# Kernel tuning notes

Measured on AMD Instinct MI355X. Metric: run time of the kernel, lower is better.

Reference implementation:

```python
import jax, jax.numpy as jnp
import numpy as np

B, S, IN, H, D, STATE, PRED = 256, 512, 32, 256, 32, 4, 96


def setup_inputs() -> dict:
    key = jax.random.key(0)
    ks = jax.random.split(key, 16)
    sc = 1.0 / np.sqrt(H)

    def u(k, shape):
        return jax.random.uniform(k, shape, jnp.float32, -sc, sc)

    return {
        "x": jax.random.normal(ks[0], (B, S, IN), jnp.float32),
        # GRU layer 0
        "W_ih_l0": u(ks[1], (3 * H, IN)),
        "W_hh_l0": u(ks[2], (3 * H, H)),
        "b_ih_l0": u(ks[3], (3 * H,)),
        "b_hh_l0": u(ks[4], (3 * H,)),
        # GRU layer 1
        "W_ih_l1": u(ks[5], (3 * H, H)),
        "W_hh_l1": u(ks[6], (3 * H, H)),
        "b_ih_l1": u(ks[7], (3 * H,)),
        "b_hh_l1": u(ks[8], (3 * H,)),
        # state projection: hidden -> STATE*output_dim
        "W_proj": u(ks[9], (STATE * D, H)),
        "b_proj": u(ks[10], (STATE * D,)),
        # observation matrix, eye-initialized (output_dim, STATE)
        "C": jnp.eye(D, STATE, dtype=jnp.float32),
        "raw_level_decay": jnp.zeros((D,), jnp.float32),
        "raw_trend_decay": jnp.zeros((D,), jnp.float32),
        "raw_gamma": jnp.zeros((D,), jnp.float32),
        "omega": jnp.zeros((D,), jnp.float32),
    }


def _gru_layer(xs, W_ih, W_hh, b_ih, b_hh):
    # xs: (B, S, in_dim). Precompute input projections as one big GEMM.
    xp = jnp.einsum('bsi,gi->bsg', xs, W_ih) + b_ih  # (B, S, 3H)

    def step(h, xt):
        gh = h @ W_hh.T + b_hh  # (B, 3H)
        xr, xz, xn = jnp.split(xt, 3, axis=-1)
        hr, hz, hn = jnp.split(gh, 3, axis=-1)
        r = jax.nn.sigmoid(xr + hr)
        z = jax.nn.sigmoid(xz + hz)
        n = jnp.tanh(xn + r * hn)
        h_new = (1.0 - z) * n + z * h
        return h_new, h_new

    h0 = jnp.zeros((xs.shape[0], W_hh.shape[1]), xs.dtype)
    _, hs = jax.lax.scan(step, h0, jnp.swapaxes(xp, 0, 1))  # (S, B, H)
    return jnp.swapaxes(hs, 0, 1)  # (B, S, H)


def reference(x, W_ih_l0, W_hh_l0, b_ih_l0, b_hh_l0,
              W_ih_l1, W_hh_l1, b_ih_l1, b_hh_l1,
              W_proj, b_proj, C,
              raw_level_decay, raw_trend_decay, raw_gamma, omega):
    h1 = _gru_layer(x, W_ih_l0, W_hh_l0, b_ih_l0, b_hh_l0)
    h2 = _gru_layer(h1, W_ih_l1, W_hh_l1, b_ih_l1, b_hh_l1)
    final_h = h2[:, -1, :]  # (B, H)

    d_out = C.shape[0]
    s = (final_h @ W_proj.T + b_proj).reshape(x.shape[0], d_out, STATE)  # (B, D, 4)

    # time-invariant block-diagonal transition coefficients
    a_l = jax.nn.sigmoid(raw_level_decay) * 0.15 + 0.85
    a_t = jax.nn.sigmoid(raw_trend_decay) * 0.25 + 0.7
    g = jax.nn.sigmoid(raw_gamma) * 0.2 + 0.8
    c, sn = jnp.cos(omega), jnp.sin(omega)
    rot00, rot01 = g * c, -g * sn
    rot10, rot11 = g * sn, g * c

    def step(s, _):
        new_s = jnp.stack([
            s[..., 0] * a_l,
            s[..., 1] * a_t,
            s[..., 2] * rot00 + s[..., 3] * rot10,
            s[..., 2] * rot01 + s[..., 3] * rot11,
        ], axis=-1)
        y = jnp.einsum('ds,bds->bd', C, new_s)
        return new_s, y

    _, ys = jax.lax.scan(step, s, None, length=PRED)  # (PRED, B, D)
    return jnp.swapaxes(ys, 0, 1)  # (B, PRED, D)
```

## Files before the change

### kernel.cpp

```cpp
#include <hip/hip_runtime.h>
#include <cstdio>
#include <cstdint>

typedef _Float16 f16;
typedef f16 hf2   __attribute__((ext_vector_type(2)));
typedef f16 f16x8 __attribute__((ext_vector_type(8)));
typedef float f32x4 __attribute__((ext_vector_type(4)));
typedef unsigned int   u32;
typedef unsigned short u16;

#define B_    256
#define S_    512
#define IN_   32
#define H_    256
#define G3_   768
#define D_    32
#define PRED_ 96
#define TC_   32
#define KPAD_ 72

#if __has_builtin(__builtin_amdgcn_fdot2)
__device__ __forceinline__ float fdot2(hf2 a, hf2 b, float c) {
  return __builtin_amdgcn_fdot2(a, b, c, false);
}
#else
__device__ __forceinline__ float fdot2(hf2 a, hf2 b, float c) {
  return c + (float)a[0] * (float)b[0] + (float)a[1] * (float)b[1];
}
#endif

__device__ __forceinline__ float sigm(float x) {
  return __builtin_amdgcn_rcpf(1.f + __expf(-x));
}
__device__ __forceinline__ float tanh_fast(float x) {
  return 1.f - 2.f * __builtin_amdgcn_rcpf(__expf(2.f * x) + 1.f);
}
__device__ __forceinline__ hf2 bc2(u32 v) { return __builtin_bit_cast(hf2, v); }

__global__ void f32_to_f16_k(const float* __restrict__ in, f16* __restrict__ out, int n) {
  int i = blockIdx.x * blockDim.x + threadIdx.x;
  if (i < n) out[i] = (f16)in[i];
}

__global__ void make_bias(const float* __restrict__ bih, const float* __restrict__ bhh,
                          float* __restrict__ out) {
  int i = blockIdx.x * blockDim.x + threadIdx.x;
  if (i < G3_) out[i] = bih[i] + (i < 512 ? bhh[i] : 0.f);
}

__device__ __forceinline__ f16x8 cvt8(const float* p) {
  float4 lo = ((const float4*)p)[0];
  float4 hi = ((const float4*)p)[1];
  f16x8 r;
  r[0] = (f16)lo.x; r[1] = (f16)lo.y; r[2] = (f16)lo.z; r[3] = (f16)lo.w;
  r[4] = (f16)hi.x; r[5] = (f16)hi.y; r[6] = (f16)hi.z; r[7] = (f16)hi.w;
  return r;
}

template <int KK>
__global__ __launch_bounds__(256) void gemm_xp(
    const void* __restrict__ Asrc, size_t aBlk, int tl_rows,
    const f16* __restrict__ Wih,
    const float* __restrict__ biasc,
    u16* __restrict__ xp) {
  const int tid = threadIdx.x;
  const int wv = tid >> 6, lane = tid & 63, lm = lane & 15, q = lane >> 4;
  const int tiles_pb = tl_rows >> 6;
  const int b = blockIdx.x / tiles_pb, hf = blockIdx.x % tiles_pb;
  const size_t arow0 = (size_t)b * aBlk + (size_t)(hf * 64) * KK;
  const size_t orow0 = (size_t)b * tl_rows + hf * 64;

#pragma unroll 1
  for (int nt = 0; nt < 12; ++nt) {
    const int n0 = wv * 192 + nt * 16;
    const f16* Bp = Wih + (size_t)(n0 + lm) * KK + q * 8;
    f32x4 acc[4];
#pragma unroll
    for (int j = 0; j < 4; ++j) acc[j] = f32x4{0.f, 0.f, 0.f, 0.f};
#pragma unroll
    for (int k0 = 0; k0 < KK; k0 += 32) {
      f16x8 bv = *(const f16x8*)(Bp + k0);
#pragma unroll
      for (int j = 0; j < 4; ++j) {
        f16x8 av;
        if constexpr (KK == 32) {
          av = cvt8((const float*)Asrc + arow0 + (size_t)(j * 16 + lm) * KK + k0 + q * 8);
        } else {
          av = *(const f16x8*)((const f16*)Asrc + arow0 + (size_t)(j * 16 + lm) * KK + k0 + q * 8);
        }
        acc[j] = __builtin_amdgcn_mfma_f32_16x16x32_f16(av, bv, acc[j], 0, 0, 0);
      }
    }
    const float bb = biasc[n0 + lm];
#pragma unroll
    for (int j = 0; j < 4; ++j)
#pragma unroll
      for (int r = 0; r < 4; ++r)
        xp[(orow0 + j * 16 + q * 4 + r) * G3_ + n0 + lm] =
            __builtin_bit_cast(u16, (f16)(acc[j][r] + bb));
  }
}

template <int LAYER>
__global__ __attribute__((amdgpu_flat_work_group_size(1024, 1024)))
__attribute__((amdgpu_waves_per_eu(4, 4))) void gru_rec(
    const u16* __restrict__ xp,
    const f16* __restrict__ Whh16,
    const float* __restrict__ bhh,
    float* __restrict__ hstate,
    f16* __restrict__ h1c,
    int tl_rows, int first) {
  const int b   = blockIdx.x;
  const int tid = threadIdx.x;
  const int p = tid >> 2, kh = tid & 3;

  uint4 w[24];
  const uint4* wsrc = (const uint4*)Whh16 + (size_t)p * 32 + kh * 8;
#pragma unroll
  for (int g = 0; g < 3; ++g)
#pragma unroll
    for (int u = 0; u < 8; ++u)
      w[g * 8 + u] = wsrc[g * 8192 + u];
  const float bhn = bhh[512 + p];

  __shared__ u16 xbuf[2][TC_ * G3_];
  __shared__ __align__(16) u16 hbuf[2][4 * KPAD_];
  __shared__ u16 hhist[TC_ * H_];

  float h = first ? 0.f : hstate[b * H_ + p];
  if (kh == 0)
    hbuf[0][(p >> 6) * KPAD_ + (p & 63)] = __builtin_bit_cast(u16, (f16)h);
  int cur = 0;
  const uint4* xsrc = (const uint4*)xp + (size_t)b * tl_rows * 96;
  const int nsub = tl_rows >> 5;

#pragma unroll 1
  for (int c2 = 0; c2 < nsub; ++c2) {
    {
      const uint4* src = xsrc + (size_t)c2 * 3072;
      uint4 v0 = src[tid], v1 = src[1024 + tid], v2 = src[2048 + tid];
      uint4* dst = (uint4*)xbuf[c2 & 1];
      dst[tid] = v0; dst[1024 + tid] = v1; dst[2048 + tid] = v2;
    }
    __syncthreads();
    const u16* xrow0 = xbuf[c2 & 1];

#pragma unroll 1
    for (int tl = 0; tl < TC_; ++tl) {
      const uint4* hb = (const uint4*)((const u16*)hbuf[cur] + kh * KPAD_);
      float ar = 0.f, az = 0.f, an = 0.f;
#pragma unroll
      for (int cc = 0; cc < 8; ++cc) {
        uint4 hv = hb[cc];
        uint4 w0 = w[cc], w1 = w[8 + cc], w2 = w[16 + cc];
        ar = fdot2(bc2(w0.x), bc2(hv.x), ar);
        az = fdot2(bc2(w1.x), bc2(hv.x), az);
        an = fdot2(bc2(w2.x), bc2(hv.x), an);
        ar = fdot2(bc2(w0.y), bc2(hv.y), ar);
        az = fdot2(bc2(w1.y), bc2(hv.y), az);
        an = fdot2(bc2(w2.y), bc2(hv.y), an);
        ar = fdot2(bc2(w0.z), bc2(hv.z), ar);
        az = fdot2(bc2(w1.z), bc2(hv.z), az);
        an = fdot2(bc2(w2.z), bc2(hv.z), an);
        ar = fdot2(bc2(w0.w), bc2(hv.w), ar);
        az = fdot2(bc2(w1.w), bc2(hv.w), az);
        an = fdot2(bc2(w2.w), bc2(hv.w), an);
      }
      ar += __shfl_xor(ar, 1); ar += __shfl_xor(ar, 2);
      az += __shfl_xor(az, 1); az += __shfl_xor(az, 2);
      an += __shfl_xor(an, 1); an += __shfl_xor(an, 2);

      const u16* xrow = xrow0 + tl * G3_;
      float xr = (float)__builtin_bit_cast(f16, xrow[p]);
      float xz = (float)__builtin_bit_cast(f16, xrow[256 + p]);
      float xn = (float)__builtin_bit_cast(f16, xrow[512 + p]);
      float r = sigm(xr + ar);
      float z = sigm(xz + az);
      float n = tanh_fast(xn + r * (an + bhn));
      h = n + z * (h - n);

      if (kh == 0) {
        u16 h16v = __builtin_bit_cast(u16, (f16)h);
        hbuf[cur ^ 1][(p >> 6) * KPAD_ + (p & 63)] = h16v;
        if constexpr (LAYER == 0) hhist[tl * H_ + p] = h16v;
      }
      __syncthreads();
      cur ^= 1;
    }

    if constexpr (LAYER == 0) {
      uint4 hv = ((const uint4*)hhist)[tid];
      ((uint4*)(h1c + ((size_t)b * tl_rows + c2 * TC_) * H_))[tid] = hv;
    }
  }
  if (kh == 0) hstate[b * H_ + p] = h;
}

__global__ __launch_bounds__(128) void proj_rollout(
    const float* __restrict__ hfinal, const float* __restrict__ Wp,
    const float* __restrict__ bp, const float* __restrict__ Cm,
    const float* __restrict__ rld, const float* __restrict__ rtd,
    const float* __restrict__ rg, const float* __restrict__ om,
    float* __restrict__ out) {
  const int b = blockIdx.x, tid = threadIdx.x;
  __shared__ float fh[256];
  __shared__ float sb[128];
  ((float2*)fh)[tid] = ((const float2*)(hfinal + b * 256))[tid];
  __syncthreads();
  const float4* wrow = (const float4*)(Wp + tid * 256);
  float acc = 0.f;
#pragma unroll 16
  for (int k4 = 0; k4 < 64; k4++) {
    float4 wv = wrow[k4];
    acc += wv.x * fh[4 * k4] + wv.y * fh[4 * k4 + 1] + wv.z * fh[4 * k4 + 2] +
           wv.w * fh[4 * k4 + 3];
  }
  sb[tid] = acc + bp[tid];
  __syncthreads();
  if (tid < 32) {
    const int dd = tid;
    float s0 = sb[dd * 4], s1 = sb[dd * 4 + 1], s2 = sb[dd * 4 + 2], s3 = sb[dd * 4 + 3];
    float al = sigm(rld[dd]) * 0.15f + 0.85f;
    float at = sigm(rtd[dd]) * 0.25f + 0.70f;
    float g  = sigm(rg[dd]) * 0.20f + 0.80f;
    float cw = cosf(om[dd]), sw = sinf(om[dd]);
    float r00 = g * cw, r01 = -g * sw, r10 = g * sw, r11 = g * cw;
    float c0 = Cm[dd * 4], c1 = Cm[dd * 4 + 1], c2 = Cm[dd * 4 + 2], c3 = Cm[dd * 4 + 3];
    float* op = out + (size_t)b * PRED_ * D_ + dd;
    for (int t = 0; t < PRED_; t++) {
      float n0 = s0 * al, n1 = s1 * at;
      float n2 = s2 * r00 + s3 * r10;
      float n3 = s2 * r01 + s3 * r11;
      op[(size_t)t * D_] = c0 * n0 + c1 * n1 + c2 * n2 + c3 * n3;
      s0 = n0; s1 = n1; s2 = n2; s3 = n3;
    }
  }
}

extern "C" void kernel_launch(void* const* d_in, const int* in_sizes, int n_in,
                              void* d_out, int out_size, void* d_ws,
                              size_t ws_size, hipStream_t stream) {
  (void)in_sizes; (void)n_in; (void)out_size;
  const float* x     = (const float*)d_in[0];
  const float* Wih0  = (const float*)d_in[1];
  const float* Whh0  = (const float*)d_in[2];
  const float* bih0  = (const float*)d_in[3];
  const float* bhh0  = (const float*)d_in[4];
  const float* Wih1  = (const float*)d_in[5];
  const float* Whh1  = (const float*)d_in[6];
  const float* bih1  = (const float*)d_in[7];
  const float* bhh1  = (const float*)d_in[8];
  const float* Wproj = (const float*)d_in[9];
  const float* bproj = (const float*)d_in[10];
  const float* Cm    = (const float*)d_in[11];
  const float* rld   = (const float*)d_in[12];
  const float* rtd   = (const float*)d_in[13];
  const float* rg    = (const float*)d_in[14];
  const float* om    = (const float*)d_in[15];
  float* out = (float*)d_out;

  char* ws = (char*)d_ws;
  const size_t wi0_off  = 0;
  const size_t wi1_off  = 49152;
  const size_t whh0_off = 442368;
  const size_t whh1_off = 835584;
  const size_t b0_off   = 1228800;
  const size_t b1_off   = 1231872;
  const size_t hs0_off  = 1234944;
  const size_t hs1_off  = 1497088;
  const size_t h1c_off  = 1759232;
  const size_t need64  = h1c_off + (size_t)B_ * 64 * H_ * 2  + (size_t)B_ * 64 * G3_ * 2;
  const size_t need128 = h1c_off + (size_t)B_ * 128 * H_ * 2 + (size_t)B_ * 128 * G3_ * 2;

  if (ws_size < need64) {
    fprintf(stderr, "kernel_launch: ws too small: have %zu need %zu — skipping\n",
            ws_size, need64);
    return;
  }
  const int TL = (ws_size >= need128) ? 128 : 64;
  const size_t xpc_off = h1c_off + (size_t)B_ * TL * H_ * 2;

  f16* wi016   = (f16*)(ws + wi0_off);
  f16* wi116   = (f16*)(ws + wi1_off);
  f16* whh016  = (f16*)(ws + whh0_off);
  f16* whh116  = (f16*)(ws + whh1_off);
  float* bias0 = (float*)(ws + b0_off);
  float* bias1 = (float*)(ws + b1_off);
  float* hst0  = (float*)(ws + hs0_off);
  float* hst1  = (float*)(ws + hs1_off);
  f16* h1c     = (f16*)(ws + h1c_off);
  u16* xpc     = (u16*)(ws + xpc_off);

  f32_to_f16_k<<<96, 256, 0, stream>>>(Wih0, wi016, G3_ * IN_);
  f32_to_f16_k<<<768, 256, 0, stream>>>(Wih1, wi116, G3_ * H_);
  f32_to_f16_k<<<768, 256, 0, stream>>>(Whh0, whh016, G3_ * H_);
  f32_to_f16_k<<<768, 256, 0, stream>>>(Whh1, whh116, G3_ * H_);
  make_bias<<<3, 256, 0, stream>>>(bih0, bhh0, bias0);
  make_bias<<<3, 256, 0, stream>>>(bih1, bhh1, bias1);

  const int nchunks = S_ / TL;
  const int gblocks = B_ * (TL / 64);
  for (int c = 0; c < nchunks; ++c) {
    gemm_xp<IN_><<<gblocks, 256, 0, stream>>>(
        (const void*)(x + (size_t)c * TL * IN_), (size_t)S_ * IN_, TL, wi016, bias0, xpc);
    gru_rec<0><<<B_, 1024, 0, stream>>>(xpc, whh016, bhh0, hst0, h1c, TL, c == 0);
    gemm_xp<H_><<<gblocks, 256, 0, stream>>>(
        (const void*)h1c, (size_t)TL * H_, TL, wi116, bias1, xpc);
    gru_rec<1><<<B_, 1024, 0, stream>>>(xpc, whh116, bhh1, hst1, nullptr, TL, c == 0);
  }
  proj_rollout<<<B_, 128, 0, stream>>>(hst1, Wproj, bproj, Cm, rld, rtd, rg, om, out);
}
```

Measured before the change: 1.687 ms.

## Halve GRU recurrence block to 512 threads with 2-way K split

Each hidden unit is now handled by 2 threads instead of 4, each holding half of the unit's recurrent weight row (48 uint4 registers instead of 24), with blocks of 512 threads. This removes one shuffle stage per gate and halves the number of waves meeting at each per-step barrier. Two independent accumulator chains per gate are added to shorten dependency latency. The cost is double the weight registers per thread, which risks spills or lower occupancy, and the padded h buffer layout is replaced by a plain contiguous one, which may bring LDS bank conflicts.

```diff
diff --git a/kernel.cpp b/kernel.cpp
--- a/kernel.cpp
+++ b/kernel.cpp
@@ -17,7 +17,6 @@
 #define D_    32
 #define PRED_ 96
 #define TC_   32
-#define KPAD_ 72
 
 #if __has_builtin(__builtin_amdgcn_fdot2)
 __device__ __forceinline__ float fdot2(hf2 a, hf2 b, float c) {
@@ -102,8 +101,7 @@
 }
 
 template <int LAYER>
-__global__ __attribute__((amdgpu_flat_work_group_size(1024, 1024)))
-__attribute__((amdgpu_waves_per_eu(4, 4))) void gru_rec(
+__global__ __launch_bounds__(512, 2) void gru_rec(
     const u16* __restrict__ xp,
     const f16* __restrict__ Whh16,
     const float* __restrict__ bhh,
@@ -112,24 +110,23 @@
     int tl_rows, int first) {
   const int b   = blockIdx.x;
   const int tid = threadIdx.x;
-  const int p = tid >> 2, kh = tid & 3;
-
-  uint4 w[24];
-  const uint4* wsrc = (const uint4*)Whh16 + (size_t)p * 32 + kh * 8;
+  const int p = tid >> 1, kh = tid & 1;
+
+  uint4 w[48];
+  const uint4* wsrc = (const uint4*)Whh16 + (size_t)p * 32 + kh * 16;
 #pragma unroll
   for (int g = 0; g < 3; ++g)
 #pragma unroll
-    for (int u = 0; u < 8; ++u)
-      w[g * 8 + u] = wsrc[g * 8192 + u];
+    for (int u = 0; u < 16; ++u)
+      w[g * 16 + u] = wsrc[g * 8192 + u];
   const float bhn = bhh[512 + p];
 
   __shared__ u16 xbuf[2][TC_ * G3_];
-  __shared__ __align__(16) u16 hbuf[2][4 * KPAD_];
+  __shared__ __align__(16) u16 hbuf[2][H_];
   __shared__ u16 hhist[TC_ * H_];
 
   float h = first ? 0.f : hstate[b * H_ + p];
-  if (kh == 0)
-    hbuf[0][(p >> 6) * KPAD_ + (p & 63)] = __builtin_bit_cast(u16, (f16)h);
+  if (kh == 0) hbuf[0][p] = __builtin_bit_cast(u16, (f16)h);
   int cur = 0;
   const uint4* xsrc = (const uint4*)xp + (size_t)b * tl_rows * 96;
   const int nsub = tl_rows >> 5;
@@ -138,37 +135,40 @@
   for (int c2 = 0; c2 < nsub; ++c2) {
     {
       const uint4* src = xsrc + (size_t)c2 * 3072;
-      uint4 v0 = src[tid], v1 = src[1024 + tid], v2 = src[2048 + tid];
+      uint4 v0 = src[tid],        v1 = src[512 + tid],  v2 = src[1024 + tid];
+      uint4 v3 = src[1536 + tid], v4 = src[2048 + tid], v5 = src[2560 + tid];
       uint4* dst = (uint4*)xbuf[c2 & 1];
-      dst[tid] = v0; dst[1024 + tid] = v1; dst[2048 + tid] = v2;
+      dst[tid] = v0;        dst[512 + tid] = v1;  dst[1024 + tid] = v2;
+      dst[1536 + tid] = v3; dst[2048 + tid] = v4; dst[2560 + tid] = v5;
     }
     __syncthreads();
     const u16* xrow0 = xbuf[c2 & 1];
 
 #pragma unroll 1
     for (int tl = 0; tl < TC_; ++tl) {
-      const uint4* hb = (const uint4*)((const u16*)hbuf[cur] + kh * KPAD_);
-      float ar = 0.f, az = 0.f, an = 0.f;
-#pragma unroll
-      for (int cc = 0; cc < 8; ++cc) {
+      const uint4* hb = (const uint4*)(hbuf[cur] + kh * 128);
+      float ar = 0.f, az = 0.f, an = 0.f, ar2 = 0.f, az2 = 0.f, an2 = 0.f;
+#pragma unroll
+      for (int cc = 0; cc < 16; ++cc) {
         uint4 hv = hb[cc];
-        uint4 w0 = w[cc], w1 = w[8 + cc], w2 = w[16 + cc];
-        ar = fdot2(bc2(w0.x), bc2(hv.x), ar);
-        az = fdot2(bc2(w1.x), bc2(hv.x), az);
-        an = fdot2(bc2(w2.x), bc2(hv.x), an);
-        ar = fdot2(bc2(w0.y), bc2(hv.y), ar);
-        az = fdot2(bc2(w1.y), bc2(hv.y), az);
-        an = fdot2(bc2(w2.y), bc2(hv.y), an);
-        ar = fdot2(bc2(w0.z), bc2(hv.z), ar);
-        az = fdot2(bc2(w1.z), bc2(hv.z), az);
-        an = fdot2(bc2(w2.z), bc2(hv.z), an);
-        ar = fdot2(bc2(w0.w), bc2(hv.w), ar);
-        az = fdot2(bc2(w1.w), bc2(hv.w), az);
-        an = fdot2(bc2(w2.w), bc2(hv.w), an);
+        uint4 w0 = w[cc], w1 = w[16 + cc], w2 = w[32 + cc];
+        ar  = fdot2(bc2(w0.x), bc2(hv.x), ar);
+        az  = fdot2(bc2(w1.x), bc2(hv.x), az);
+        an  = fdot2(bc2(w2.x), bc2(hv.x), an);
+        ar2 = fdot2(bc2(w0.y), bc2(hv.y), ar2);
+        az2 = fdot2(bc2(w1.y), bc2(hv.y), az2);
+        an2 = fdot2(bc2(w2.y), bc2(hv.y), an2);
+        ar  = fdot2(bc2(w0.z), bc2(hv.z), ar);
+        az  = fdot2(bc2(w1.z), bc2(hv.z), az);
+        an  = fdot2(bc2(w2.z), bc2(hv.z), an);
+        ar2 = fdot2(bc2(w0.w), bc2(hv.w), ar2);
+        az2 = fdot2(bc2(w1.w), bc2(hv.w), az2);
+        an2 = fdot2(bc2(w2.w), bc2(hv.w), an2);
       }
-      ar += __shfl_xor(ar, 1); ar += __shfl_xor(ar, 2);
-      az += __shfl_xor(az, 1); az += __shfl_xor(az, 2);
-      an += __shfl_xor(an, 1); an += __shfl_xor(an, 2);
+      ar += ar2; az += az2; an += an2;
+      ar += __shfl_xor(ar, 1);
+      az += __shfl_xor(az, 1);
+      an += __shfl_xor(an, 1);
 
       const u16* xrow = xrow0 + tl * G3_;
       float xr = (float)__builtin_bit_cast(f16, xrow[p]);
@@ -181,7 +181,7 @@
 
       if (kh == 0) {
         u16 h16v = __builtin_bit_cast(u16, (f16)h);
-        hbuf[cur ^ 1][(p >> 6) * KPAD_ + (p & 63)] = h16v;
+        hbuf[cur ^ 1][p] = h16v;
         if constexpr (LAYER == 0) hhist[tl * H_ + p] = h16v;
       }
       __syncthreads();
@@ -189,8 +189,11 @@
     }
 
     if constexpr (LAYER == 0) {
-      uint4 hv = ((const uint4*)hhist)[tid];
-      ((uint4*)(h1c + ((size_t)b * tl_rows + c2 * TC_) * H_))[tid] = hv;
+      uint4 hv0 = ((const uint4*)hhist)[tid];
+      uint4 hv1 = ((const uint4*)hhist)[512 + tid];
+      uint4* dst = (uint4*)(h1c + ((size_t)b * tl_rows + c2 * TC_) * H_);
+      dst[tid] = hv0;
+      dst[512 + tid] = hv1;
     }
   }
   if (kh == 0) hstate[b * H_ + p] = h;
@@ -303,10 +306,10 @@
   for (int c = 0; c < nchunks; ++c) {
     gemm_xp<IN_><<<gblocks, 256, 0, stream>>>(
         (const void*)(x + (size_t)c * TL * IN_), (size_t)S_ * IN_, TL, wi016, bias0, xpc);
-    gru_rec<0><<<B_, 1024, 0, stream>>>(xpc, whh016, bhh0, hst0, h1c, TL, c == 0);
+    gru_rec<0><<<B_, 512, 0, stream>>>(xpc, whh016, bhh0, hst0, h1c, TL, c == 0);
     gemm_xp<H_><<<gblocks, 256, 0, stream>>>(
         (const void*)h1c, (size_t)TL * H_, TL, wi116, bias1, xpc);
-    gru_rec<1><<<B_, 1024, 0, stream>>>(xpc, whh116, bhh1, hst1, nullptr, TL, c == 0);
+    gru_rec<1><<<B_, 512, 0, stream>>>(xpc, whh116, bhh1, hst1, nullptr, TL, c == 0);
   }
   proj_rollout<<<B_, 128, 0, stream>>>(hst1, Wproj, bproj, Cm, rld, rtd, rg, om, out);
 }
```

Measured after the change: 1.555 ms. -7.8%, faster.

## Batch 16 sequences per block and compute GRU recurrence with MFMA

Applied to the files above, without the earlier changes.

Replaces the per-sequence fdot2 recurrent kernel with one where each block processes 16 batch rows and computes the hidden-to-hidden matvec as 16x16x32 MFMA tiles with weights held in registers. Input projections are staged four timesteps at a time into LDS and layer-0 outputs are written directly to global. This aims to use matrix cores instead of scalar dot products, but launches only 16 blocks, leaving most CUs idle and lengthening per-step dependent MFMA chains.

```diff
diff --git a/kernel.cpp b/kernel.cpp
--- a/kernel.cpp
+++ b/kernel.cpp
@@ -16,18 +16,7 @@
 #define G3_   768
 #define D_    32
 #define PRED_ 96
-#define TC_   32
-#define KPAD_ 72
-
-#if __has_builtin(__builtin_amdgcn_fdot2)
-__device__ __forceinline__ float fdot2(hf2 a, hf2 b, float c) {
-  return __builtin_amdgcn_fdot2(a, b, c, false);
-}
-#else
-__device__ __forceinline__ float fdot2(hf2 a, hf2 b, float c) {
-  return c + (float)a[0] * (float)b[0] + (float)a[1] * (float)b[1];
-}
-#endif
+#define XBPAD_ 776
 
 __device__ __forceinline__ float sigm(float x) {
   return __builtin_amdgcn_rcpf(1.f + __expf(-x));
@@ -35,7 +24,6 @@
 __device__ __forceinline__ float tanh_fast(float x) {
   return 1.f - 2.f * __builtin_amdgcn_rcpf(__expf(2.f * x) + 1.f);
 }
-__device__ __forceinline__ hf2 bc2(u32 v) { return __builtin_bit_cast(hf2, v); }
 
 __global__ void f32_to_f16_k(const float* __restrict__ in, f16* __restrict__ out, int n) {
   int i = blockIdx.x * blockDim.x + threadIdx.x;
@@ -102,98 +90,120 @@
 }
 
 template <int LAYER>
-__global__ __attribute__((amdgpu_flat_work_group_size(1024, 1024)))
-__attribute__((amdgpu_waves_per_eu(4, 4))) void gru_rec(
+__global__ __launch_bounds__(512, 2) void gru_rec_mfma(
     const u16* __restrict__ xp,
     const f16* __restrict__ Whh16,
     const float* __restrict__ bhh,
     float* __restrict__ hstate,
     f16* __restrict__ h1c,
-    int tl_rows, int first) {
-  const int b   = blockIdx.x;
+    int TL, int first) {
   const int tid = threadIdx.x;
-  const int p = tid >> 2, kh = tid & 3;
-
-  uint4 w[24];
-  const uint4* wsrc = (const uint4*)Whh16 + (size_t)p * 32 + kh * 8;
-#pragma unroll
-  for (int g = 0; g < 3; ++g)
-#pragma unroll
-    for (int u = 0; u < 8; ++u)
-      w[g * 8 + u] = wsrc[g * 8192 + u];
-  const float bhn = bhh[512 + p];
-
-  __shared__ u16 xbuf[2][TC_ * G3_];
-  __shared__ __align__(16) u16 hbuf[2][4 * KPAD_];
-  __shared__ u16 hhist[TC_ * H_];
-
-  float h = first ? 0.f : hstate[b * H_ + p];
-  if (kh == 0)
-    hbuf[0][(p >> 6) * KPAD_ + (p & 63)] = __builtin_bit_cast(u16, (f16)h);
+  const int wv = tid >> 6, lane = tid & 63, lm = lane & 15, q = lane >> 4;
+  const int b0 = blockIdx.x * 16;
+
+  f16x8 bf[2][3][8];
+#pragma unroll
+  for (int t2 = 0; t2 < 2; ++t2)
+#pragma unroll
+    for (int g = 0; g < 3; ++g)
+#pragma unroll
+      for (int kf = 0; kf < 8; ++kf) {
+        const int u = wv * 32 + t2 * 16 + lm;
+        bf[t2][g][kf] =
+            *(const f16x8*)(Whh16 + (size_t)(g * 256 + u) * 256 + kf * 32 + q * 8);
+      }
+  float bhn[2];
+  bhn[0] = bhh[512 + wv * 32 + lm];
+  bhn[1] = bhh[512 + wv * 32 + 16 + lm];
+
+  __shared__ __align__(16) u16 hlds[2][16][264];
+  __shared__ __align__(16) u16 xb[4][16][XBPAD_];
+
+  float hreg[8];
+#pragma unroll
+  for (int t2 = 0; t2 < 2; ++t2)
+#pragma unroll
+    for (int r = 0; r < 4; ++r) {
+      const int row = q * 4 + r, u = wv * 32 + t2 * 16 + lm;
+      float hv = first ? 0.f : hstate[(size_t)(b0 + row) * 256 + u];
+      hreg[t2 * 4 + r] = hv;
+      hlds[0][row][u] = __builtin_bit_cast(u16, (f16)hv);
+    }
   int cur = 0;
-  const uint4* xsrc = (const uint4*)xp + (size_t)b * tl_rows * 96;
-  const int nsub = tl_rows >> 5;
+  const uint4* gsrc = (const uint4*)xp;
 
 #pragma unroll 1
-  for (int c2 = 0; c2 < nsub; ++c2) {
-    {
-      const uint4* src = xsrc + (size_t)c2 * 3072;
-      uint4 v0 = src[tid], v1 = src[1024 + tid], v2 = src[2048 + tid];
-      uint4* dst = (uint4*)xbuf[c2 & 1];
-      dst[tid] = v0; dst[1024 + tid] = v1; dst[2048 + tid] = v2;
+  for (int t0 = 0; t0 < TL; t0 += 4) {
+#pragma unroll
+    for (int pass = 0; pass < 4; ++pass) {
+      uint4 v[3];
+#pragma unroll
+      for (int i = 0; i < 3; ++i) {
+        const int idx = (pass * 3 + i) * 512 + tid;
+        const int oh = idx * 8;
+        const int s = oh / 12288, rem = oh - s * 12288;
+        const int row = rem / 768, u = rem - row * 768;
+        v[i] = gsrc[(((size_t)(b0 + row) * TL + (t0 + s)) * G3_ + u) >> 3];
+      }
+#pragma unroll
+      for (int i = 0; i < 3; ++i) {
+        const int idx = (pass * 3 + i) * 512 + tid;
+        const int oh = idx * 8;
+        const int s = oh / 12288, rem = oh - s * 12288;
+        const int row = rem / 768, u = rem - row * 768;
+        *(uint4*)(&xb[s][row][u]) = v[i];
+      }
     }
     __syncthreads();
-    const u16* xrow0 = xbuf[c2 & 1];
 
 #pragma unroll 1
-    for (int tl = 0; tl < TC_; ++tl) {
-      const uint4* hb = (const uint4*)((const u16*)hbuf[cur] + kh * KPAD_);
-      float ar = 0.f, az = 0.f, an = 0.f;
-#pragma unroll
-      for (int cc = 0; cc < 8; ++cc) {
-        uint4 hv = hb[cc];
-        uint4 w0 = w[cc], w1 = w[8 + cc], w2 = w[16 + cc];
-        ar = fdot2(bc2(w0.x), bc2(hv.x), ar);
-        az = fdot2(bc2(w1.x), bc2(hv.x), az);
-        an = fdot2(bc2(w2.x), bc2(hv.x), an);
-        ar = fdot2(bc2(w0.y), bc2(hv.y), ar);
-        az = fdot2(bc2(w1.y), bc2(hv.y), az);
-        an = fdot2(bc2(w2.y), bc2(hv.y), an);
-        ar = fdot2(bc2(w0.z), bc2(hv.z), ar);
-        az = fdot2(bc2(w1.z), bc2(hv.z), az);
-        an = fdot2(bc2(w2.z), bc2(hv.z), an);
-        ar = fdot2(bc2(w0.w), bc2(hv.w), ar);
-        az = fdot2(bc2(w1.w), bc2(hv.w), az);
-        an = fdot2(bc2(w2.w), bc2(hv.w), an);
-      }
-      ar += __shfl_xor(ar, 1); ar += __shfl_xor(ar, 2);
-      az += __shfl_xor(az, 1); az += __shfl_xor(az, 2);
-      an += __shfl_xor(an, 1); an += __shfl_xor(an, 2);
-
-      const u16* xrow = xrow0 + tl * G3_;
-      float xr = (float)__builtin_bit_cast(f16, xrow[p]);
-      float xz = (float)__builtin_bit_cast(f16, xrow[256 + p]);
-      float xn = (float)__builtin_bit_cast(f16, xrow[512 + p]);
-      float r = sigm(xr + ar);
-      float z = sigm(xz + az);
-      float n = tanh_fast(xn + r * (an + bhn));
-      h = n + z * (h - n);
-
-      if (kh == 0) {
-        u16 h16v = __builtin_bit_cast(u16, (f16)h);
-        hbuf[cur ^ 1][(p >> 6) * KPAD_ + (p & 63)] = h16v;
-        if constexpr (LAYER == 0) hhist[tl * H_ + p] = h16v;
+    for (int s = 0; s < 4; ++s) {
+#pragma unroll
+      for (int t2 = 0; t2 < 2; ++t2) {
+        f32x4 aR = {0.f, 0.f, 0.f, 0.f}, aZ = aR, aN = aR;
+#pragma unroll
+        for (int kh = 0; kh < 2; ++kh) {
+          f16x8 af[4];
+#pragma unroll
+          for (int kf = 0; kf < 4; ++kf)
+            af[kf] = *(const f16x8*)(&hlds[cur][lm][(kh * 4 + kf) * 32 + q * 8]);
+#pragma unroll
+          for (int kf = 0; kf < 4; ++kf) {
+            aR = __builtin_amdgcn_mfma_f32_16x16x32_f16(af[kf], bf[t2][0][kh * 4 + kf], aR, 0, 0, 0);
+            aZ = __builtin_amdgcn_mfma_f32_16x16x32_f16(af[kf], bf[t2][1][kh * 4 + kf], aZ, 0, 0, 0);
+            aN = __builtin_amdgcn_mfma_f32_16x16x32_f16(af[kf], bf[t2][2][kh * 4 + kf], aN, 0, 0, 0);
+          }
+        }
+        const int u = wv * 32 + t2 * 16 + lm;
+#pragma unroll
+        for (int r = 0; r < 4; ++r) {
+          const int row = q * 4 + r;
+          float xr = (float)*(const f16*)&xb[s][row][u];
+          float xz = (float)*(const f16*)&xb[s][row][256 + u];
+          float xn = (float)*(const f16*)&xb[s][row][512 + u];
+          float rr = sigm(xr + aR[r]);
+          float zz = sigm(xz + aZ[r]);
+          float nn = tanh_fast(xn + rr * (aN[r] + bhn[t2]));
+          float hv = nn + zz * (hreg[t2 * 4 + r] - nn);
+          hreg[t2 * 4 + r] = hv;
+          const u16 h16v = __builtin_bit_cast(u16, (f16)hv);
+          hlds[cur ^ 1][row][u] = h16v;
+          if constexpr (LAYER == 0)
+            h1c[((size_t)(b0 + row) * TL + (t0 + s)) * H_ + u] = __builtin_bit_cast(f16, h16v);
+        }
       }
       __syncthreads();
       cur ^= 1;
     }
-
-    if constexpr (LAYER == 0) {
-      uint4 hv = ((const uint4*)hhist)[tid];
-      ((uint4*)(h1c + ((size_t)b * tl_rows + c2 * TC_) * H_))[tid] = hv;
-    }
-  }
-  if (kh == 0) hstate[b * H_ + p] = h;
+  }
+
+#pragma unroll
+  for (int t2 = 0; t2 < 2; ++t2)
+#pragma unroll
+    for (int r = 0; r < 4; ++r) {
+      const int row = q * 4 + r, u = wv * 32 + t2 * 16 + lm;
+      hstate[(size_t)(b0 + row) * 256 + u] = hreg[t2 * 4 + r];
+    }
 }
 
 __global__ __launch_bounds__(128) void proj_rollout(
@@ -303,10 +313,10 @@
   for (int c = 0; c < nchunks; ++c) {
     gemm_xp<IN_><<<gblocks, 256, 0, stream>>>(
         (const void*)(x + (size_t)c * TL * IN_), (size_t)S_ * IN_, TL, wi016, bias0, xpc);
-    gru_rec<0><<<B_, 1024, 0, stream>>>(xpc, whh016, bhh0, hst0, h1c, TL, c == 0);
+    gru_rec_mfma<0><<<16, 512, 0, stream>>>(xpc, whh016, bhh0, hst0, h1c, TL, c == 0);
     gemm_xp<H_><<<gblocks, 256, 0, stream>>>(
         (const void*)h1c, (size_t)TL * H_, TL, wi116, bias1, xpc);
-    gru_rec<1><<<B_, 1024, 0, stream>>>(xpc, whh116, bhh1, hst1, nullptr, TL, c == 0);
+    gru_rec_mfma<1><<<16, 512, 0, stream>>>(xpc, whh116, bhh1, hst1, nullptr, TL, c == 0);
   }
   proj_rollout<<<B_, 128, 0, stream>>>(hst1, Wproj, bproj, Cm, rld, rtd, rg, om, out);
 }
```

After: 3.257 ms. 1.93x slower.
